# Kernel tuning notes

Hardware: AMD Instinct MI355X
Metric: run time of the kernel (lower is better)

Reference implementation:

```python
import jax, jax.numpy as jnp
import numpy as np

B, S, H = 8, 8192, 1024
CAPACITY_FACTOR = 0.5


def setup_inputs() -> dict:
    key = jax.random.key(0)
    ks = jax.random.split(key, 5)
    sc = lambda fan: np.float32(1.0 / np.sqrt(fan))
    return {
        "x": jax.random.normal(ks[0], (B, S, H), dtype=jnp.float32),
        # router: Linear(H, H//4) -> ReLU -> Linear(H//4, 1)
        "W1": jax.random.normal(ks[1], (H, H // 4), dtype=jnp.float32) * sc(H),
        "b1": jnp.zeros((H // 4,), dtype=jnp.float32),
        "W2": jax.random.normal(ks[2], (H // 4, 1), dtype=jnp.float32) * sc(H // 4),
        "b2": jnp.zeros((1,), dtype=jnp.float32),
        # external layer_fn realized as a dense layer: gelu(x @ Wl)
        "Wl": jax.random.normal(ks[3], (H, H), dtype=jnp.float32) * sc(H),
    }


def reference(x, W1, b1, W2, b2, Wl):
    # router scores [B, S, 1]
    scores = jax.nn.relu(jnp.einsum("bsh,hd->bsd", x, W1) + b1)
    scores = jnp.einsum("bsd,do->bso", scores, W2) + b2
    routing_weights = jax.nn.sigmoid(scores)  # [B, S, 1]

    # eval path: process only top-capacity tokens per batch row
    capacity = int(S * CAPACITY_FACTOR)
    _, top_idx = jax.lax.top_k(scores[..., 0], capacity)  # [B, C]

    selected = jnp.take_along_axis(x, top_idx[..., None], axis=1)  # [B, C, H]
    processed = jax.nn.gelu(jnp.einsum("bch,hd->bcd", selected, Wl))  # layer_fn

    batch_idx = jnp.arange(x.shape[0])[:, None]  # [B, 1]
    output = x.at[batch_idx, top_idx].set(processed)  # scatter back into clone of x
    return output, routing_weights
```

## Files before the change

### kernel.cpp

```cpp
#include <hip/hip_runtime.h>
#include <stdint.h>

#define B_   8
#define S_   8192
#define H_   1024
#define HQ_  256
#define CAP_ 4096
#define UCAP_ (S_-CAP_)
#define M_   (B_*CAP_)
#define EPSB 0.012f
#define LCAP 8192

using f32x4 = __attribute__((ext_vector_type(4))) float;
using s16x8 = __attribute__((ext_vector_type(8))) short;

__device__ __forceinline__ unsigned short f2bf(float f) {
  unsigned u = __float_as_uint(f);
  u += 0x7FFF + ((u >> 16) & 1);
  return (unsigned short)(u >> 16);
}
__device__ __forceinline__ float bf2f(unsigned short h) {
  return __uint_as_float(((unsigned)h) << 16);
}

__device__ __forceinline__ float gelu_f(float v) {
  float s = v + 0.044715f * v * v * v;
  float e = __expf(-1.5957691216057308f * s);
  return v * __builtin_amdgcn_rcpf(1.0f + e);
}

__device__ __forceinline__ unsigned mono(float f) {
  unsigned u = __float_as_uint(f);
  return (u & 0x80000000u) ? ~u : (u | 0x80000000u);
}
__device__ __forceinline__ float unmono(unsigned k) {
  unsigned u = (k & 0x80000000u) ? (k & 0x7fffffffu) : ~k;
  return __uint_as_float(u);
}

__device__ __forceinline__ void gload_lds16(const void* g, void* l) {
  __builtin_amdgcn_global_load_lds(
      (const __attribute__((address_space(1))) void*)(uintptr_t)g,
      (__attribute__((address_space(3))) void*)(uintptr_t)l,
      16, 0, 0);
}

__device__ __forceinline__ float radix_select_T(
    const float* __restrict__ srow, unsigned* hist,
    unsigned* sh_b, unsigned* sh_gt, int tid) {
  unsigned prefix = 0; int plen = 0; unsigned rank = CAP_;
  #pragma unroll
  for (int round = 0; round < 3; ++round) {
    const int nb = (round < 2) ? 11 : 10;
    hist[tid] = 0; hist[tid + 1024] = 0;
    __syncthreads();
    for (int i = tid; i < S_; i += 1024) {
      unsigned k = mono(srow[i]);
      if (plen == 0 || (k >> (32 - plen)) == prefix) {
        unsigned bucket = (k << plen) >> (32 - nb);
        atomicAdd(&hist[bucket], 1u);
      }
    }
    __syncthreads();
    for (int s = 1; s < 2048; s <<= 1) {
      unsigned t0 = (tid + s < 2048) ? hist[tid + s] : 0;
      unsigned t1 = (tid + 1024 + s < 2048) ? hist[tid + 1024 + s] : 0;
      __syncthreads();
      hist[tid] += t0; hist[tid + 1024] += t1;
      __syncthreads();
    }
    #pragma unroll
    for (int h = 0; h < 2; ++h) {
      int i = tid + h * 1024;
      unsigned ge = hist[i];
      unsigned gt = (i < 2047) ? hist[i + 1] : 0;
      if (gt < rank && rank <= ge) { *sh_b = (unsigned)i; *sh_gt = gt; }
    }
    __syncthreads();
    prefix = (prefix << nb) | *sh_b;
    plen += nb;
    rank -= *sh_gt;
    __syncthreads();
  }
  return unmono(prefix);
}

__global__ __launch_bounds__(256) void prep_kernel(
    const float* __restrict__ W1, unsigned short* __restrict__ w1t_hi,
    const float* __restrict__ wl, unsigned short* __restrict__ wlt) {
  __shared__ float tile[32][33];
  const int bid = blockIdx.x;
  const int tx = threadIdx.x, ty = threadIdx.y;
  if (bid < 256) {
    int n0 = (bid & 7) * 32, k0 = (bid >> 3) * 32;
    for (int i = ty; i < 32; i += 8) tile[i][tx] = W1[(size_t)(k0 + i) * HQ_ + n0 + tx];
    __syncthreads();
    for (int i = ty; i < 32; i += 8)
      w1t_hi[(size_t)(n0 + i) * H_ + k0 + tx] = f2bf(tile[tx][i]);
  } else {
    int idx = bid - 256;
    int x0 = (idx & 31) * 32, y0 = (idx >> 5) * 32;
    for (int i = ty; i < 32; i += 8) tile[i][tx] = wl[(size_t)(y0 + i) * H_ + x0 + tx];
    __syncthreads();
    for (int i = ty; i < 32; i += 8)
      wlt[(size_t)(x0 + i) * H_ + y0 + tx] = f2bf(tile[tx][i]);
  }
}

__global__ __launch_bounds__(256) void router_mfma_kernel(
    const float* __restrict__ x, const unsigned short* __restrict__ w1t_hi,
    const float* __restrict__ b1, const float* __restrict__ W2,
    const float* __restrict__ b2, float* __restrict__ scores,
    float* __restrict__ rw, int* __restrict__ count) {
  __shared__ __align__(16) float Af[64 * 64];
  __shared__ __align__(16) unsigned short Bs[256 * 64];
  __shared__ float part[64][4];
  const int t = threadIdx.x;
  const int lane = t & 63, w = t >> 6;
  const int m0 = blockIdx.x * 64;
  if (blockIdx.x == 0 && t == 0) *count = 0;
  const int r16 = lane & 15, ks = lane >> 4;

  const float* aP[4];
  int adst[4];
  #pragma unroll
  for (int u = 0; u < 4; ++u) {
    int c = u * 256 + t;
    int row = c >> 4, q = c & 15;
    int qz = q ^ (row & 15);
    aP[u] = x + (size_t)(m0 + row) * H_ + qz * 4;
    adst[u] = c * 4;
  }
  const unsigned short* bP[8];
  int bdst[8];
  #pragma unroll
  for (int u = 0; u < 8; ++u) {
    int c = u * 256 + t;
    int row = c >> 3, sl = c & 7;
    int slz = sl ^ (row & 7);
    bP[u] = w1t_hi + (size_t)row * H_ + slz * 8;
    bdst[u] = c * 8;
  }

  f32x4 acc[4][4];
  #pragma unroll
  for (int i = 0; i < 4; ++i)
    #pragma unroll
    for (int j = 0; j < 4; ++j) acc[i][j] = (f32x4){0.f, 0.f, 0.f, 0.f};

  for (int k0 = 0; k0 < H_; k0 += 64) {
    #pragma unroll
    for (int u = 0; u < 4; ++u) gload_lds16(aP[u] + k0, &Af[adst[u]]);
    #pragma unroll
    for (int u = 0; u < 8; ++u) gload_lds16(bP[u] + k0, &Bs[bdst[u]]);
    __syncthreads();
    s16x8 af[4][2], bfr[4][2];
    #pragma unroll
    for (int i = 0; i < 4; ++i)
      #pragma unroll
      for (int kk = 0; kk < 2; ++kk) {
        int r_ = i * 16 + r16;
        int g2 = 2 * (kk * 4 + ks);
        float4 f0 = *(const float4*)&Af[(r_ * 16 + (g2 ^ (r_ & 15))) * 4];
        float4 f1 = *(const float4*)&Af[(r_ * 16 + ((g2 + 1) ^ (r_ & 15))) * 4];
        unsigned short hh[8];
        hh[0] = f2bf(f0.x); hh[1] = f2bf(f0.y); hh[2] = f2bf(f0.z); hh[3] = f2bf(f0.w);
        hh[4] = f2bf(f1.x); hh[5] = f2bf(f1.y); hh[6] = f2bf(f1.z); hh[7] = f2bf(f1.w);
        af[i][kk] = *(s16x8*)hh;
      }
    #pragma unroll
    for (int j = 0; j < 4; ++j)
      #pragma unroll
      for (int kk = 0; kk < 2; ++kk) {
        int r_ = w * 64 + j * 16 + r16;
        bfr[j][kk] = *(const s16x8*)&Bs[r_ * 64 + ((kk * 4 + ks) ^ (r_ & 7)) * 8];
      }
    #pragma unroll
    for (int i = 0; i < 4; ++i)
      #pragma unroll
      for (int j = 0; j < 4; ++j)
        #pragma unroll
        for (int kk = 0; kk < 2; ++kk)
          acc[i][j] = __builtin_amdgcn_mfma_f32_16x16x32_bf16(
              af[i][kk], bfr[j][kk], acc[i][j], 0, 0, 0);
    __syncthreads();
  }

  float b1v[4], w2v[4];
  #pragma unroll
  for (int j = 0; j < 4; ++j) {
    int n = w * 64 + j * 16 + r16;
    b1v[j] = b1[n]; w2v[j] = W2[n];
  }
  const int g4 = lane >> 4;
  #pragma unroll
  for (int i = 0; i < 4; ++i) {
    #pragma unroll
    for (int r = 0; r < 4; ++r) {
      float p = 0.f;
      #pragma unroll
      for (int j = 0; j < 4; ++j) {
        float h = acc[i][j][r] + b1v[j];
        h = fmaxf(h, 0.f);
        p = fmaf(h, w2v[j], p);
      }
      p += __shfl_xor(p, 1);
      p += __shfl_xor(p, 2);
      p += __shfl_xor(p, 4);
      p += __shfl_xor(p, 8);
      if (r16 == 0) part[i * 16 + g4 * 4 + r][w] = p;
    }
  }
  __syncthreads();
  if (t < 64) {
    float sc = part[t][0] + part[t][1] + part[t][2] + part[t][3] + b2[0];
    scores[m0 + t] = sc;
    rw[m0 + t] = 1.f / (1.f + expf(-sc));
  }
}

__global__ __launch_bounds__(1024) void select_band_kernel(
    const float* __restrict__ scores, int* __restrict__ list,
    int* __restrict__ count) {
  __shared__ unsigned hist[2048];
  __shared__ unsigned sh_b, sh_gt;
  const int b = blockIdx.x;
  const int tid = threadIdx.x;
  const float* srow = scores + (size_t)b * S_;
  const float T = radix_select_T(srow, hist, &sh_b, &sh_gt, tid);
  for (int i = tid; i < S_; i += 1024) {
    float s = srow[i];
    if (fabsf(s - T) <= EPSB) {
      int p = atomicAdd(count, 1);
      if (p < LCAP) list[p] = b * S_ + i;
    }
  }
}

__global__ __launch_bounds__(256) void recompute_kernel(
    const float* __restrict__ x, const float* __restrict__ W1,
    const float* __restrict__ b1, const float* __restrict__ W2,
    const float* __restrict__ b2, const int* __restrict__ list,
    const int* __restrict__ count, float* __restrict__ scores,
    float* __restrict__ rw) {
  __shared__ float xr[4][H_];
  __shared__ float red[4][4];
  int n = *count; if (n > LCAP) n = LCAP;
  const int j = threadIdx.x;
  for (int base = blockIdx.x * 4; base < n; base += gridDim.x * 4) {
    int nt = n - base; if (nt > 4) nt = 4;
    for (int tt = 0; tt < 4; ++tt) {
      int tok = list[base + ((tt < nt) ? tt : 0)];
      const float* xrow = x + (size_t)tok * H_;
      for (int k = j; k < H_; k += 256) xr[tt][k] = xrow[k];
    }
    __syncthreads();
    float a0 = 0.f, a1 = 0.f, a2 = 0.f, a3 = 0.f;
    for (int k = 0; k < H_; ++k) {
      float wv = W1[(size_t)k * HQ_ + j];
      a0 = fmaf(xr[0][k], wv, a0);
      a1 = fmaf(xr[1][k], wv, a1);
      a2 = fmaf(xr[2][k], wv, a2);
      a3 = fmaf(xr[3][k], wv, a3);
    }
    float aa[4] = {a0, a1, a2, a3};
    #pragma unroll
    for (int tt = 0; tt < 4; ++tt) {
      float h = fmaxf(aa[tt] + b1[j], 0.f);
      float v = h * W2[j];
      v += __shfl_xor(v, 1);  v += __shfl_xor(v, 2);  v += __shfl_xor(v, 4);
      v += __shfl_xor(v, 8);  v += __shfl_xor(v, 16); v += __shfl_xor(v, 32);
      if ((j & 63) == 0) red[tt][j >> 6] = v;
    }
    __syncthreads();
    if (j < nt) {
      int tok = list[base + j];
      float sc = red[j][0] + red[j][1] + red[j][2] + red[j][3] + b2[0];
      scores[tok] = sc;
      rw[tok] = 1.f / (1.f + expf(-sc));
    }
    __syncthreads();
  }
}

__global__ __launch_bounds__(1024) void compact_kernel(
    const float* __restrict__ scores, int* __restrict__ comp,
    int* __restrict__ ucomp) {
  __shared__ unsigned hist[2048];
  __shared__ unsigned sh_b, sh_gt;
  __shared__ int wc_eq[16], wc_sel[16], red[16];
  const int b = blockIdx.x;
  const float* srow = scores + (size_t)b * S_;
  const int tid = threadIdx.x, lane = tid & 63, wid = tid >> 6;
  const float T = radix_select_T(srow, hist, &sh_b, &sh_gt, tid);

  int cgt = 0;
  #pragma unroll
  for (int c = 0; c < 8; ++c) cgt += (srow[c * 1024 + tid] > T) ? 1 : 0;
  cgt += __shfl_xor(cgt, 1);  cgt += __shfl_xor(cgt, 2);  cgt += __shfl_xor(cgt, 4);
  cgt += __shfl_xor(cgt, 8);  cgt += __shfl_xor(cgt, 16); cgt += __shfl_xor(cgt, 32);
  if (lane == 0) red[wid] = cgt;
  __syncthreads();
  int cnt_gt = 0;
  #pragma unroll
  for (int i = 0; i < 16; ++i) cnt_gt += red[i];
  const int need = CAP_ - cnt_gt;

  int* crow = comp + b * CAP_;
  int* urow = ucomp + b * UCAP_;
  int sel_base = 0, unsel_base = 0, eq_base = 0;
  __syncthreads();
  for (int c = 0; c < 8; ++c) {
    int idx = c * 1024 + tid;
    float s = srow[idx];
    bool gt = s > T, eq = (s == T);
    unsigned long long meq = __ballot(eq);
    if (lane == 0) wc_eq[wid] = __popcll(meq);
    __syncthreads();
    int eq_off = eq_base, eq_tot = 0;
    #pragma unroll
    for (int w2 = 0; w2 < 16; ++w2) { if (w2 < wid) eq_off += wc_eq[w2]; eq_tot += wc_eq[w2]; }
    int eqpos = eq_off + __popcll(meq & ((1ull << lane) - 1));
    bool take = gt || (eq && eqpos < need);
    unsigned long long mt = __ballot(take);
    if (lane == 0) wc_sel[wid] = __popcll(mt);
    __syncthreads();
    int sel_off = sel_base, sel_tot = 0;
    #pragma unroll
    for (int w2 = 0; w2 < 16; ++w2) { if (w2 < wid) sel_off += wc_sel[w2]; sel_tot += wc_sel[w2]; }
    if (take) {
      crow[sel_off + __popcll(mt & ((1ull << lane) - 1))] = idx;
    } else {
      int un_off = unsel_base + wid * 64 - (sel_off - sel_base);
      urow[un_off + __popcll(~mt & ((1ull << lane) - 1))] = idx;
    }
    sel_base += sel_tot; unsel_base += 1024 - sel_tot; eq_base += eq_tot;
    __syncthreads();
  }
}

__global__ __launch_bounds__(256) void gather_copy_kernel(
    const float* __restrict__ x, const int* __restrict__ comp,
    const int* __restrict__ ucomp, unsigned short* __restrict__ xg,
    float* __restrict__ out) {
  const int bid = blockIdx.x;
  const int tx = threadIdx.x;
  if (bid < M_) {
    int b = bid >> 12, cc = bid & (CAP_ - 1);
    int token = comp[b * CAP_ + cc];
    float4 v = ((const float4*)(x + ((size_t)(b * S_ + token)) * H_))[tx];
    ushort4 o;
    o.x = f2bf(v.x); o.y = f2bf(v.y); o.z = f2bf(v.z); o.w = f2bf(v.w);
    *(ushort4*)&xg[(size_t)bid * H_ + tx * 4] = o;
  } else {
    int i = bid - M_;
    int b = i >> 12, r = i & (UCAP_ - 1);
    int token = ucomp[b * UCAP_ + r];
    size_t row = (size_t)b * S_ + token;
    ((float4*)(out + row * H_))[tx] = ((const float4*)(x + row * H_))[tx];
  }
}

#define ISSUE_A(P, KT, BUF) do {                                               \
    int row_ = half * 128 + (P) * 32 + rr;                                     \
    int slz_ = sl ^ (row_ & 7);                                                \
    gload_lds16(xg + (size_t)(m0 + row_) * H_ + (KT) * 64 + slz_ * 8,          \
                &As[BUF][row_ * 64 + sl * 8]);                                 \
  } while (0)
#define ISSUE_B(P, KT, BUF) do {                                               \
    int row_ = half * 128 + (P) * 32 + rr;                                     \
    int slz_ = sl ^ (row_ & 7);                                                \
    gload_lds16(wlt + (size_t)(n0 + row_) * H_ + (KT) * 64 + slz_ * 8,         \
                &Bs[BUF][row_ * 64 + sl * 8]);                                 \
  } while (0)
#define MOE_PHASE(P, ISSUE, WAITSTR) do {                                      \
    s16x8 af[2][2];                                                            \
    _Pragma("unroll")                                                          \
    for (int i = 0; i < 2; ++i)                                                \
      _Pragma("unroll")                                                        \
      for (int kk = 0; kk < 2; ++kk) {                                         \
        int r_ = wr * 128 + (2 * (P) + i) * 16 + r16;                          \
        af[i][kk] = *(const s16x8*)&As[c_][r_ * 64 + ((kk * 4 + ks) ^ (r_ & 7)) * 8]; \
      }                                                                        \
    if ((P) == 0) {                                                            \
      _Pragma("unroll")                                                        \
      for (int j = 0; j < 4; ++j)                                              \
        _Pragma("unroll")                                                      \
        for (int kk = 0; kk < 2; ++kk) {                                       \
          int r_ = wc * 64 + j * 16 + r16;                                     \
          bfr[j][kk] = *(const s16x8*)&Bs[c_][r_ * 64 + ((kk * 4 + ks) ^ (r_ & 7)) * 8]; \
        }                                                                      \
    }                                                                          \
    ISSUE                                                                      \
    __builtin_amdgcn_s_barrier();                                              \
    asm volatile("s_waitcnt lgkmcnt(0)" ::: "memory");                         \
    __builtin_amdgcn_sched_barrier(0);                                         \
    __builtin_amdgcn_s_setprio(1);                                             \
    _Pragma("unroll")                                                          \
    for (int i = 0; i < 2; ++i)                                                \
      _Pragma("unroll")                                                        \
      for (int j = 0; j < 4; ++j)                                              \
        _Pragma("unroll")                                                      \
        for (int kk = 0; kk < 2; ++kk)                                         \
          acc[2 * (P) + i][j] = __builtin_amdgcn_mfma_f32_16x16x32_bf16(       \
              af[i][kk], bfr[j][kk], acc[2 * (P) + i][j], 0, 0, 0);            \
    __builtin_amdgcn_s_setprio(0);                                             \
    __builtin_amdgcn_sched_barrier(0);                                         \
    asm volatile("s_waitcnt " WAITSTR ::: "memory");                           \
    __builtin_amdgcn_s_barrier();                                              \
    __builtin_amdgcn_sched_barrier(0);                                         \
  } while (0)

__global__ __launch_bounds__(512, 1) void moe_gemm_kernel(
    const unsigned short* __restrict__ xg, const unsigned short* __restrict__ wlt,
    const int* __restrict__ comp, float* __restrict__ out) {
  __shared__ __align__(16) unsigned short As[2][256 * 64];
  __shared__ __align__(16) unsigned short Bs[2][256 * 64];
  __shared__ int toks[256];
  const int t = threadIdx.x;
  const int lane = t & 63, w = t >> 6;
  const int bid = blockIdx.x;
  const int xcd = bid & 7, wb = bid >> 3;
  const int m0 = (xcd * 16 + (wb >> 2)) * 256;
  const int n0 = (wb & 3) * 256;
  const int bb = m0 >> 12;
  if (t < 256) toks[t] = comp[bb * CAP_ + (m0 & (CAP_ - 1)) + t];
  const int wr = w >> 2, wc = w & 3;
  const int r16 = lane & 15, ks = lane >> 4;
  const int half = t >> 8, rr = (t >> 3) & 31, sl = t & 7;

  f32x4 acc[8][4];
  #pragma unroll
  for (int i = 0; i < 8; ++i)
    #pragma unroll
    for (int j = 0; j < 4; ++j) acc[i][j] = (f32x4){0.f, 0.f, 0.f, 0.f};

  ISSUE_B(0, 0, 0); ISSUE_B(1, 0, 0); ISSUE_B(2, 0, 0); ISSUE_B(3, 0, 0);
  ISSUE_A(0, 0, 0); ISSUE_A(1, 0, 0); ISSUE_A(2, 0, 0); ISSUE_A(3, 0, 0);
  asm volatile("s_waitcnt vmcnt(3)" ::: "memory");
  __syncthreads();

  for (int kt = 0; kt < 15; ++kt) {
    const int c_ = kt & 1, nb_ = c_ ^ 1;
    const int kn = kt + 1;
    s16x8 bfr[4][2];
    MOE_PHASE(0, { ISSUE_B(0, kn, nb_); ISSUE_B(1, kn, nb_); }, "vmcnt(4)");
    MOE_PHASE(1, { ISSUE_B(2, kn, nb_); ISSUE_B(3, kn, nb_); }, "vmcnt(5)");
    MOE_PHASE(2, { ISSUE_A(0, kn, nb_); ISSUE_A(1, kn, nb_); }, "vmcnt(6)");
    MOE_PHASE(3, { ISSUE_A(2, kn, nb_); ISSUE_A(3, kn, nb_); }, "vmcnt(3)");
  }
  {
    const int c_ = 1;
    s16x8 bfr[4][2];
    MOE_PHASE(0, {;}, "vmcnt(2)");
    MOE_PHASE(1, {;}, "vmcnt(1)");
    MOE_PHASE(2, {;}, "vmcnt(0)");
    MOE_PHASE(3, {;}, "vmcnt(63)");
  }

  const int g4 = lane >> 4;
  #pragma unroll
  for (int i = 0; i < 8; ++i) {
    #pragma unroll
    for (int r = 0; r < 4; ++r) {
      int rl = wr * 128 + i * 16 + g4 * 4 + r;
      int token = toks[rl];
      float* orow = out + ((size_t)(bb * S_ + token)) * H_ + n0 + wc * 64;
      #pragma unroll
      for (int j = 0; j < 4; ++j)
        orow[j * 16 + r16] = gelu_f(acc[i][j][r]);
    }
  }
}

extern "C" void kernel_launch(void* const* d_in, const int* in_sizes, int n_in,
                              void* d_out, int out_size, void* d_ws, size_t ws_size,
                              hipStream_t stream) {
  const float* x  = (const float*)d_in[0];
  const float* W1 = (const float*)d_in[1];
  const float* b1 = (const float*)d_in[2];
  const float* W2 = (const float*)d_in[3];
  const float* b2 = (const float*)d_in[4];
  const float* Wl = (const float*)d_in[5];
  float* out = (float*)d_out;
  float* rw  = out + (size_t)B_ * S_ * H_;

  char* ws = (char*)d_ws;
  float* scores        = (float*)ws;
  int*   comp          = (int*)(ws + (256 << 10));
  int*   count         = (int*)(ws + (384 << 10) + 256);
  int*   list          = (int*)(ws + (384 << 10) + 512);
  int*   ucomp         = (int*)(ws + (448 << 10));
  unsigned short* wlt  = (unsigned short*)(ws + (1 << 20));
  unsigned short* xg   = (unsigned short*)(ws + (3 << 20));
  unsigned short* w1t_hi = xg;

  hipLaunchKernelGGL(prep_kernel, dim3(1280), dim3(32, 8), 0, stream,
                     W1, w1t_hi, Wl, wlt);
  hipLaunchKernelGGL(router_mfma_kernel, dim3((B_*S_)/64), dim3(256), 0, stream,
                     x, w1t_hi, b1, W2, b2, scores, rw, count);
  hipLaunchKernelGGL(select_band_kernel, dim3(B_), dim3(1024), 0, stream,
                     scores, list, count);
  hipLaunchKernelGGL(recompute_kernel, dim3(128), dim3(256), 0, stream,
                     x, W1, b1, W2, b2, list, count, scores, rw);
  hipLaunchKernelGGL(compact_kernel, dim3(B_), dim3(1024), 0, stream,
                     scores, comp, ucomp);
  hipLaunchKernelGGL(gather_copy_kernel, dim3(M_ + B_*UCAP_), dim3(256), 0, stream,
                     x, comp, ucomp, xg, out);
  hipLaunchKernelGGL(moe_gemm_kernel, dim3((M_/256)*(H_/256)), dim3(512), 0, stream,
                     xg, wlt, comp, out);
}
```

Measured before the change: 422.9 us.

## Restructure router GEMM so each wave owns 16 rows across all N

The router kernel stops staging x through LDS. Each wave now loads its own 16 rows of x straight from global memory into registers and computes all 256 hidden columns. This removes the A-tile LDS traffic, the cross-wave partial-sum array and one barrier, and launch bounds now ask for 4 blocks per CU. In exchange, each wave reads every B fragment (4x more LDS reads of W1), loads x uncoalesced per lane, and holds 16 accumulators; the recompute kernel grid is also doubled.

```diff
diff --git a/kernel.cpp b/kernel.cpp
--- a/kernel.cpp
+++ b/kernel.cpp
@@ -107,30 +107,20 @@
   }
 }
 
-__global__ __launch_bounds__(256) void router_mfma_kernel(
+__global__ __launch_bounds__(256, 4) void router_mfma_kernel(
     const float* __restrict__ x, const unsigned short* __restrict__ w1t_hi,
     const float* __restrict__ b1, const float* __restrict__ W2,
     const float* __restrict__ b2, float* __restrict__ scores,
     float* __restrict__ rw, int* __restrict__ count) {
-  __shared__ __align__(16) float Af[64 * 64];
   __shared__ __align__(16) unsigned short Bs[256 * 64];
-  __shared__ float part[64][4];
   const int t = threadIdx.x;
   const int lane = t & 63, w = t >> 6;
   const int m0 = blockIdx.x * 64;
   if (blockIdx.x == 0 && t == 0) *count = 0;
   const int r16 = lane & 15, ks = lane >> 4;
 
-  const float* aP[4];
-  int adst[4];
-  #pragma unroll
-  for (int u = 0; u < 4; ++u) {
-    int c = u * 256 + t;
-    int row = c >> 4, q = c & 15;
-    int qz = q ^ (row & 15);
-    aP[u] = x + (size_t)(m0 + row) * H_ + qz * 4;
-    adst[u] = c * 4;
-  }
+  const float* arow = x + (size_t)(m0 + w * 16 + r16) * H_ + ks * 8;
+
   const unsigned short* bP[8];
   int bdst[8];
   #pragma unroll
@@ -142,80 +132,56 @@
     bdst[u] = c * 8;
   }
 
-  f32x4 acc[4][4];
-  #pragma unroll
-  for (int i = 0; i < 4; ++i)
-    #pragma unroll
-    for (int j = 0; j < 4; ++j) acc[i][j] = (f32x4){0.f, 0.f, 0.f, 0.f};
+  f32x4 acc[16];
+  #pragma unroll
+  for (int j = 0; j < 16; ++j) acc[j] = (f32x4){0.f, 0.f, 0.f, 0.f};
 
   for (int k0 = 0; k0 < H_; k0 += 64) {
     #pragma unroll
-    for (int u = 0; u < 4; ++u) gload_lds16(aP[u] + k0, &Af[adst[u]]);
-    #pragma unroll
     for (int u = 0; u < 8; ++u) gload_lds16(bP[u] + k0, &Bs[bdst[u]]);
     __syncthreads();
-    s16x8 af[4][2], bfr[4][2];
-    #pragma unroll
-    for (int i = 0; i < 4; ++i)
+    #pragma unroll
+    for (int kk = 0; kk < 2; ++kk) {
+      float4 a0 = *(const float4*)(arow + k0 + kk * 32);
+      float4 a1 = *(const float4*)(arow + k0 + kk * 32 + 4);
+      unsigned short hh[8];
+      hh[0] = f2bf(a0.x); hh[1] = f2bf(a0.y); hh[2] = f2bf(a0.z); hh[3] = f2bf(a0.w);
+      hh[4] = f2bf(a1.x); hh[5] = f2bf(a1.y); hh[6] = f2bf(a1.z); hh[7] = f2bf(a1.w);
+      s16x8 af = *(s16x8*)hh;
       #pragma unroll
-      for (int kk = 0; kk < 2; ++kk) {
-        int r_ = i * 16 + r16;
-        int g2 = 2 * (kk * 4 + ks);
-        float4 f0 = *(const float4*)&Af[(r_ * 16 + (g2 ^ (r_ & 15))) * 4];
-        float4 f1 = *(const float4*)&Af[(r_ * 16 + ((g2 + 1) ^ (r_ & 15))) * 4];
-        unsigned short hh[8];
-        hh[0] = f2bf(f0.x); hh[1] = f2bf(f0.y); hh[2] = f2bf(f0.z); hh[3] = f2bf(f0.w);
-        hh[4] = f2bf(f1.x); hh[5] = f2bf(f1.y); hh[6] = f2bf(f1.z); hh[7] = f2bf(f1.w);
-        af[i][kk] = *(s16x8*)hh;
+      for (int j = 0; j < 16; ++j) {
+        int rn = j * 16 + r16;
+        s16x8 bf = *(const s16x8*)&Bs[rn * 64 + ((kk * 4 + ks) ^ (rn & 7)) * 8];
+        acc[j] = __builtin_amdgcn_mfma_f32_16x16x32_bf16(af, bf, acc[j], 0, 0, 0);
       }
-    #pragma unroll
-    for (int j = 0; j < 4; ++j)
-      #pragma unroll
-      for (int kk = 0; kk < 2; ++kk) {
-        int r_ = w * 64 + j * 16 + r16;
-        bfr[j][kk] = *(const s16x8*)&Bs[r_ * 64 + ((kk * 4 + ks) ^ (r_ & 7)) * 8];
-      }
-    #pragma unroll
-    for (int i = 0; i < 4; ++i)
-      #pragma unroll
-      for (int j = 0; j < 4; ++j)
-        #pragma unroll
-        for (int kk = 0; kk < 2; ++kk)
-          acc[i][j] = __builtin_amdgcn_mfma_f32_16x16x32_bf16(
-              af[i][kk], bfr[j][kk], acc[i][j], 0, 0, 0);
-    __syncthreads();
-  }
-
-  float b1v[4], w2v[4];
-  #pragma unroll
-  for (int j = 0; j < 4; ++j) {
-    int n = w * 64 + j * 16 + r16;
+    }
+    __syncthreads();
+  }
+
+  float b1v[16], w2v[16];
+  #pragma unroll
+  for (int j = 0; j < 16; ++j) {
+    int n = j * 16 + r16;
     b1v[j] = b1[n]; w2v[j] = W2[n];
   }
-  const int g4 = lane >> 4;
-  #pragma unroll
-  for (int i = 0; i < 4; ++i) {
-    #pragma unroll
-    for (int r = 0; r < 4; ++r) {
-      float p = 0.f;
-      #pragma unroll
-      for (int j = 0; j < 4; ++j) {
-        float h = acc[i][j][r] + b1v[j];
-        h = fmaxf(h, 0.f);
-        p = fmaf(h, w2v[j], p);
-      }
-      p += __shfl_xor(p, 1);
-      p += __shfl_xor(p, 2);
-      p += __shfl_xor(p, 4);
-      p += __shfl_xor(p, 8);
-      if (r16 == 0) part[i * 16 + g4 * 4 + r][w] = p;
-    }
-  }
-  __syncthreads();
-  if (t < 64) {
-    float sc = part[t][0] + part[t][1] + part[t][2] + part[t][3] + b2[0];
-    scores[m0 + t] = sc;
-    rw[m0 + t] = 1.f / (1.f + expf(-sc));
+  const float bias2 = b2[0];
+  #pragma unroll
+  for (int r = 0; r < 4; ++r) {
+    float p = 0.f;
+    #pragma unroll
+    for (int j = 0; j < 16; ++j) {
+      float h = fmaxf(acc[j][r] + b1v[j], 0.f);
+      p = fmaf(h, w2v[j], p);
+    }
+    p += __shfl_xor(p, 1);
+    p += __shfl_xor(p, 2);
+    p += __shfl_xor(p, 4);
+    p += __shfl_xor(p, 8);
+    if (r16 == 0) {
+      int row = m0 + w * 16 + (lane >> 4) * 4 + r;
+      scores[row] = p + bias2;
+      rw[row] = 1.f / (1.f + expf(-(p + bias2)));
+    }
   }
 }
 
@@ -501,7 +467,7 @@
                      x, w1t_hi, b1, W2, b2, scores, rw, count);
   hipLaunchKernelGGL(select_band_kernel, dim3(B_), dim3(1024), 0, stream,
                      scores, list, count);
-  hipLaunchKernelGGL(recompute_kernel, dim3(128), dim3(256), 0, stream,
+  hipLaunchKernelGGL(recompute_kernel, dim3(256), dim3(256), 0, stream,
                      x, W1, b1, W2, b2, list, count, scores, rw);
   hipLaunchKernelGGL(compact_kernel, dim3(B_), dim3(1024), 0, stream,
                      scores, comp, ucomp);
```

Result: faster. 365.4 us (-13.6%).
